# Performance work log

Measured on AMD Instinct MI355X. Metric: run time of the kernel, lower is better.

Reference implementation:

```python
import jax, jax.numpy as jnp
import numpy as np

D_MODEL = 1024
NUM_HEADS = 16
HEAD_DIM = D_MODEL // NUM_HEADS


def setup_inputs() -> dict:
    key = jax.random.key(0)
    ks = jax.random.split(key, 12)
    B, Lq, Lkv = 4, 1024, 2048
    s = 1.0 / np.sqrt(D_MODEL)
    inp = {
        "decoder_hidden": jax.random.normal(ks[0], (B, Lq, D_MODEL), jnp.float32),
        "encoder_hidden": jax.random.normal(ks[1], (B, Lkv, D_MODEL), jnp.float32),
        "encoder_mask": jnp.ones((B, 1, 1, Lkv), jnp.int32),
        "Wq": jax.random.normal(ks[2], (D_MODEL, D_MODEL), jnp.float32) * s,
        "bq": jnp.zeros((D_MODEL,), jnp.float32),
        "Wk": jax.random.normal(ks[3], (D_MODEL, D_MODEL), jnp.float32) * s,
        "bk": jnp.zeros((D_MODEL,), jnp.float32),
        "Wv": jax.random.normal(ks[4], (D_MODEL, D_MODEL), jnp.float32) * s,
        "bv": jnp.zeros((D_MODEL,), jnp.float32),
        "Wo": jax.random.normal(ks[5], (D_MODEL, D_MODEL), jnp.float32) * s,
        "bo": jnp.zeros((D_MODEL,), jnp.float32),
    }
    return inp


def _split_heads(x):
    # [B, L, D] -> [B, H, L, Dh]
    B, L, _ = x.shape
    return x.reshape(B, L, NUM_HEADS, HEAD_DIM).transpose(0, 2, 1, 3)


def reference(decoder_hidden, encoder_hidden, encoder_mask,
              Wq, bq, Wk, bk, Wv, bv, Wo, bo):
    B, Lq, _ = decoder_hidden.shape
    q = _split_heads(decoder_hidden @ Wq.T + bq)   # [B,H,Lq,Dh]
    k = _split_heads(encoder_hidden @ Wk.T + bk)   # [B,H,Lkv,Dh]
    v = _split_heads(encoder_hidden @ Wv.T + bv)   # [B,H,Lkv,Dh]
    scale = 1.0 / np.sqrt(HEAD_DIM).astype(np.float32)
    scores = jnp.einsum('bhqd,bhkd->bhqk', q, k) * scale  # [B,H,Lq,Lkv]
    scores = jnp.where(encoder_mask == 0, jnp.float32(-jnp.inf), scores)
    attn = jax.nn.softmax(scores, axis=-1)  # dropout is identity in eval mode
    out = jnp.einsum('bhqk,bhkd->bhqd', attn, v)  # [B,H,Lq,Dh]
    out = out.transpose(0, 2, 1, 3).reshape(B, Lq, D_MODEL)
    return out @ Wo.T + bo
```

## Files before the change

### kernel.cpp

```cpp
#include <hip/hip_runtime.h>
#include <hip/hip_bf16.h>
#include <stdint.h>
#include <math.h>

#define B_   4
#define H_   16
#define LQ_  1024
#define LKV_ 2048
#define DM_  1024
#define DH_  64

typedef __attribute__((ext_vector_type(8))) __bf16 bf16x8;
typedef __attribute__((ext_vector_type(4))) float  f32x4;
typedef __attribute__((ext_vector_type(16))) float f32x16;
typedef __attribute__((ext_vector_type(8))) short  short8;
typedef __attribute__((ext_vector_type(2))) unsigned uint2v;

__device__ __forceinline__ void gload_lds16(const void* g, void* l) {
  __builtin_amdgcn_global_load_lds(
      (const __attribute__((address_space(1))) void*)g,
      (__attribute__((address_space(3))) void*)l, 16, 0, 0);
}

__device__ __forceinline__ void drain_vmem() {
  asm volatile("s_waitcnt vmcnt(0)" ::: "memory");
  __builtin_amdgcn_sched_barrier(0);
}

#if __has_builtin(__builtin_amdgcn_exp2f)
__device__ __forceinline__ float EXP2(float x) { return __builtin_amdgcn_exp2f(x); }
#else
__device__ __forceinline__ float EXP2(float x) {
  float r; asm("v_exp_f32 %0, %1" : "=v"(r) : "v"(x)); return r;
}
#endif

#if __has_builtin(__builtin_amdgcn_permlane32_swap)
__device__ __forceinline__ void xswap(unsigned& a, unsigned& b) {
  uint2v r = __builtin_amdgcn_permlane32_swap(a, b, false, false);
  a = r[0]; b = r[1];
}
#else
__device__ __forceinline__ void xswap(unsigned& a, unsigned& b) {
  unsigned xa = (unsigned)__shfl_xor((int)a, 32);
  unsigned xb = (unsigned)__shfl_xor((int)b, 32);
  bool hi = (threadIdx.x & 32) != 0;
  unsigned na = hi ? xb : a;
  unsigned nb = hi ? b : xa;
  a = na; b = nb;
}
#endif

__device__ __forceinline__ unsigned pack2(float a, float b) {
  unsigned lo = (unsigned)__bfloat16_as_ushort(__float2bfloat16(a));
  unsigned hi = (unsigned)__bfloat16_as_ushort(__float2bfloat16(b));
  return lo | (hi << 16);
}

struct CastArgs {
  const float* src[6];
  __hip_bfloat16* dst[6];
  int n[6];
  const int* msk;
  __hip_bfloat16* mdst;
  int mn;
};

__global__ void cast_multi(CastArgs a) {
  int seg = blockIdx.y;
  int i = (blockIdx.x * blockDim.x + threadIdx.x) * 8;
  if (seg == 6) {
    if (i >= a.mn) return;
    const int* s = a.msk + i;
    union { short8 v; __hip_bfloat16 h[8]; } u;
#pragma unroll
    for (int j = 0; j < 8; ++j) u.h[j] = __float2bfloat16(s[j] ? 1.0f : 0.0f);
    *(short8*)(a.mdst + i) = u.v;
    return;
  }
  int n = a.n[seg];
  if (i >= n) return;
  const float* s = a.src[seg] + i;
  float4 x = *(const float4*)s;
  float4 y = *(const float4*)(s + 4);
  union { short8 v; __hip_bfloat16 h[8]; } u;
  u.h[0] = __float2bfloat16(x.x); u.h[1] = __float2bfloat16(x.y);
  u.h[2] = __float2bfloat16(x.z); u.h[3] = __float2bfloat16(x.w);
  u.h[4] = __float2bfloat16(y.x); u.h[5] = __float2bfloat16(y.y);
  u.h[6] = __float2bfloat16(y.z); u.h[7] = __float2bfloat16(y.w);
  *(short8*)(a.dst[seg] + i) = u.v;
}

template<int MODE>
__global__ __launch_bounds__(256, 3)
void gemm_bt(const __hip_bfloat16* __restrict__ A,
             const __hip_bfloat16* __restrict__ Bt,
             const float* __restrict__ bias,
             void* __restrict__ Cout, int M, int N, int K) {
  __shared__ __hip_bfloat16 lA[2][128 * 64];
  __shared__ __hip_bfloat16 lB[2][64 * 64];
  const int tid = threadIdx.x;
  const int lane = tid & 63, wv = tid >> 6;
  const int l16 = lane & 15, lg = lane >> 4;
  const int wm = wv >> 1, wn = wv & 1;
  const int xcd = blockIdx.x & 7, idx = blockIdx.x >> 3;
  const int tileM = (xcd * 4 + (idx >> 4)) * 128, tileN = (idx & 15) * 64;
  const int KB = K * 2;

  f32x4 acc[4][2] = {};
  const int o0 = wv * 1024 + lane * 16;

  auto GSTAGE = [&](int bi, int kt) {
#pragma unroll
    for (int j = 0; j < 4; ++j) {
      int o = o0 + j * 4096;
      int row = o >> 7, col = (o & 127) ^ ((row & 7) << 4);
      gload_lds16((const char*)A + (size_t)(tileM + row) * KB + kt * 2 + col,
                  (char*)lA[bi] + wv * 1024 + j * 4096);
    }
#pragma unroll
    for (int j = 0; j < 2; ++j) {
      int o = o0 + j * 4096;
      int row = o >> 7, col = (o & 127) ^ ((row & 7) << 4);
      gload_lds16((const char*)Bt + (size_t)(tileN + row) * KB + kt * 2 + col,
                  (char*)lB[bi] + wv * 1024 + j * 4096);
    }
  };

  GSTAGE(0, 0);
  drain_vmem();
  __syncthreads();
  int buf = 0;
  const int NT = K / 64;
  for (int t = 0; t < NT; ++t) {
    if (t + 1 < NT) GSTAGE(buf ^ 1, (t + 1) * 64);
    bf16x8 af[4][2], bfr[2][2];
#pragma unroll
    for (int mt = 0; mt < 4; ++mt) {
      const int row = wm * 64 + mt * 16 + l16;
      const int sw = (row & 7) << 4;
#pragma unroll
      for (int kk = 0; kk < 2; ++kk)
        af[mt][kk] = *(const bf16x8*)((const char*)lA[buf] + row * 128 + ((kk * 64 + lg * 16) ^ sw));
    }
#pragma unroll
    for (int nt = 0; nt < 2; ++nt) {
      const int row = wn * 32 + nt * 16 + l16;
      const int sw = (row & 7) << 4;
#pragma unroll
      for (int kk = 0; kk < 2; ++kk)
        bfr[nt][kk] = *(const bf16x8*)((const char*)lB[buf] + row * 128 + ((kk * 64 + lg * 16) ^ sw));
    }
#pragma unroll
    for (int kk = 0; kk < 2; ++kk)
#pragma unroll
      for (int mt = 0; mt < 4; ++mt)
#pragma unroll
        for (int nt = 0; nt < 2; ++nt)
          acc[mt][nt] = __builtin_amdgcn_mfma_f32_16x16x32_bf16(af[mt][kk], bfr[nt][kk], acc[mt][nt], 0, 0, 0);
    drain_vmem();
    __syncthreads();
    buf ^= 1;
  }

#pragma unroll
  for (int mt = 0; mt < 4; ++mt) {
#pragma unroll
    for (int nt = 0; nt < 2; ++nt) {
      int col = tileN + wn * 32 + nt * 16 + l16;
      float bcol = bias[col];
      int row0 = tileM + wm * 64 + mt * 16 + lg * 4;
      f32x4 a = acc[mt][nt];
#pragma unroll
      for (int r = 0; r < 4; ++r) {
        int row = row0 + r;
        float v = a[r] + bcol;
        if (MODE == 0) {
          ((__hip_bfloat16*)Cout)[(size_t)row * N + col] = __float2bfloat16(v);
        } else {
          ((float*)Cout)[(size_t)row * N + col] = v;
        }
      }
    }
  }
}

__global__ __launch_bounds__(256, 3)
void gemm_qkv(const __hip_bfloat16* __restrict__ decB,
              const __hip_bfloat16* __restrict__ WqB,
              const float* __restrict__ bq,
              const __hip_bfloat16* __restrict__ encB,
              const __hip_bfloat16* __restrict__ WkvB,
              const float* __restrict__ bk,
              const float* __restrict__ bv,
              __hip_bfloat16* __restrict__ Qout,
              __hip_bfloat16* __restrict__ Kout,
              __hip_bfloat16* __restrict__ Vtout,
              const int* __restrict__ vmask) {
  const int K = 1024;
  __shared__ __hip_bfloat16 ls[24576];
  __hip_bfloat16* lAp = ls;
  __hip_bfloat16* lBp = ls + 12288;
  const int tid = threadIdx.x;
  const int lane = tid & 63, wv = tid >> 6;
  const int l16 = lane & 15, lg = lane >> 4;
  const int wm = wv >> 1, wn = wv & 1;

  const int xcd = blockIdx.x & 7;
  const int idx = blockIdx.x >> 3;
  const bool isQ = idx < 32;
  int tileM, tileN;
  const __hip_bfloat16 *A, *Bt;
  if (isQ) {
    int qt = xcd * 32 + idx;
    tileM = (qt >> 3) * 128; tileN = (qt & 7) * 128;
    A = decB; Bt = WqB;
  } else {
    int kvt = xcd * 128 + (idx - 32);
    tileM = (kvt >> 4) * 128; tileN = (kvt & 15) * 128;
    A = encB; Bt = WkvB;
  }
  const int KB = K * 2;

  f32x4 acc[4][4] = {};
  const int o0 = tid * 16;

  auto GSTAGE = [&](int bi, int kt) {
#pragma unroll
    for (int j = 0; j < 2; ++j) {
      int o = o0 + j * 4096;
      int row = o >> 6, col = (o & 63) ^ ((row & 3) << 4);
      gload_lds16((const char*)A + (size_t)(tileM + row) * KB + kt * 2 + col,
                  (char*)(lAp + bi * 4096) + (tid & 192) * 16 + j * 4096);
    }
#pragma unroll
    for (int j = 0; j < 2; ++j) {
      int o = o0 + j * 4096;
      int row = o >> 6, col = (o & 63) ^ ((row & 3) << 4);
      gload_lds16((const char*)Bt + (size_t)(tileN + row) * KB + kt * 2 + col,
                  (char*)(lBp + bi * 4096) + (tid & 192) * 16 + j * 4096);
    }
  };

  GSTAGE(0, 0);
  GSTAGE(1, 32);
  const int NT = K / 32;
  for (int t = 0; t < NT; ++t) {
    if (t < NT - 1) {
      asm volatile("s_waitcnt vmcnt(4)" ::: "memory");
    } else {
      asm volatile("s_waitcnt vmcnt(0)" ::: "memory");
    }
    __builtin_amdgcn_sched_barrier(0);
    __syncthreads();
    if (t + 2 < NT) GSTAGE((t + 2) % 3, (t + 2) * 32);

    const int buf = t % 3;
    bf16x8 af[4], bfr[4];
#pragma unroll
    for (int mt = 0; mt < 4; ++mt) {
      const int row = wm * 64 + mt * 16 + l16;
      af[mt] = *(const bf16x8*)((const char*)(lAp + buf * 4096) + row * 64 + ((lg * 16) ^ ((row & 3) << 4)));
    }
#pragma unroll
    for (int nt = 0; nt < 4; ++nt) {
      const int row = wn * 64 + nt * 16 + l16;
      bfr[nt] = *(const bf16x8*)((const char*)(lBp + buf * 4096) + row * 64 + ((lg * 16) ^ ((row & 3) << 4)));
    }
#pragma unroll
    for (int mt = 0; mt < 4; ++mt)
#pragma unroll
      for (int nt = 0; nt < 4; ++nt)
        acc[mt][nt] = __builtin_amdgcn_mfma_f32_16x16x32_bf16(af[mt], bfr[nt], acc[mt][nt], 0, 0, 0);
  }

  if (!isQ && tileN >= 1024) {
    const int b0 = tileM >> 11;
    const int kvb = tileM & 2047;
    const int cvbase = tileN - 1024;
    __syncthreads();
#pragma unroll
    for (int mt = 0; mt < 4; ++mt) {
      int kvr0 = wm * 64 + mt * 16 + lg * 4;
#pragma unroll
      for (int nt = 0; nt < 4; ++nt) {
        int cvr = wn * 64 + nt * 16 + l16;
        float bc = bv[cvbase + cvr];
        f32x4 a = acc[mt][nt];
        union { unsigned u2[2]; __hip_bfloat16 h[4]; } pkv;
#pragma unroll
        for (int r = 0; r < 4; ++r) {
          float v = a[r] + bc;
          if (!vmask[b0 * 2048 + kvb + kvr0 + r]) v = 0.0f;
          pkv.h[r] = __float2bfloat16(v);
        }
        *(uint2v*)(ls + cvr * 132 + kvr0) = *(uint2v*)pkv.u2;
      }
    }
    __syncthreads();
#pragma unroll
    for (int p = 0; p < 32; ++p) {
      int row = wv + p * 4;
      unsigned d = *(const unsigned*)((const char*)ls + row * 264 + lane * 4);
      *(unsigned*)((char*)Vtout + (((size_t)(b0 * 1024 + cvbase + row)) * 2048 + kvb + lane * 2) * 2) = d;
    }
  } else {
#pragma unroll
    for (int mt = 0; mt < 4; ++mt) {
#pragma unroll
      for (int nt = 0; nt < 4; ++nt) {
        int col = tileN + wn * 64 + nt * 16 + l16;
        int row0 = tileM + wm * 64 + mt * 16 + lg * 4;
        f32x4 a = acc[mt][nt];
        if (isQ) {
          float bc = bq[col];
#pragma unroll
          for (int r = 0; r < 4; ++r) {
            int row = row0 + r;
            Qout[(size_t)row * 1024 + col] = __float2bfloat16(a[r] + bc);
          }
        } else {
          float bc = bk[col];
#pragma unroll
          for (int r = 0; r < 4; ++r) {
            int row = row0 + r;
            Kout[(size_t)row * 1024 + col] = __float2bfloat16(a[r] + bc);
          }
        }
      }
    }
  }
}

__global__ __launch_bounds__(256, 2)
void attn_fwd(const __hip_bfloat16* __restrict__ Qg,
              const __hip_bfloat16* __restrict__ Kg,
              const __hip_bfloat16* __restrict__ Vt,
              const __hip_bfloat16* __restrict__ mkb,
              __hip_bfloat16* __restrict__ AO) {
  __shared__ __hip_bfloat16 lK[2][128 * 64];
  __shared__ __hip_bfloat16 lV[2][2][64 * 64];
  const int tid = threadIdx.x, lane = tid & 63, wv = tid >> 6;
  const int l32 = lane & 31, h = lane >> 5;

  const int blk = blockIdx.x;
  const int c8 = blk & 7, j = blk >> 3;
  const int g8 = c8 * 8 + (j & 7);
  const int qi = j >> 3;
  const int hd = g8 & 15, b = g8 >> 4;
  const int qb = qi * 128;
  const int q0 = qb + wv * 32;

  const char* qbase = (const char*)Qg +
      ((size_t)(b * LQ_ + q0 + l32) * DM_ + hd * DH_ + h * 8) * 2;
  bf16x8 qf[4];
#pragma unroll
  for (int dk = 0; dk < 4; ++dk) qf[dk] = *(const bf16x8*)(qbase + dk * 32);

  f32x16 o_[2] = {};
  f32x16 l_acc = {};
  float m2 = -1e30f;
  const float S2 = 0.18033688f;
  const __hip_bfloat16* mrow = mkb + b * LKV_;
  const char* Kbase = (const char*)Kg + ((size_t)(b * LKV_) * DM_ + hd * DH_) * 2;
  const char* Vbase = (const char*)Vt + ((size_t)((b * H_ + hd) * DH_)) * LKV_ * 2;

  const int ofs = wv * 1024 + lane * 16;

  auto STAGE = [&](int bi, int kv0) {
#pragma unroll
    for (int r = 0; r < 4; ++r) {
      int o = ofs + r * 4096;
      int row = o >> 7, col = (o & 127) ^ ((row & 7) << 4);
      gload_lds16(Kbase + (size_t)(kv0 + row) * 2048 + col,
                  (char*)lK[bi] + wv * 1024 + r * 4096);
    }
#pragma unroll
    for (int s = 0; s < 2; ++s)
#pragma unroll
      for (int r = 0; r < 2; ++r) {
        int o = ofs + r * 4096;
        int row = o >> 7, col = (o & 127) ^ ((row & 7) << 4);
        gload_lds16(Vbase + (size_t)row * 4096 + (kv0 + s * 64) * 2 + col,
                    (char*)lV[bi][s] + wv * 1024 + r * 4096);
      }
  };

  STAGE(0, 0);
  drain_vmem();
  __syncthreads();
  int buf = 0;

  for (int it = 0; it < LKV_ / 128; ++it) {
    const int kv0 = it * 128;
    if (it + 1 < LKV_ / 128) STAGE(buf ^ 1, kv0 + 128);

    f32x16 z[4];
#pragma unroll
    for (int t = 0; t < 4; ++t) {
      z[t] = {};
      const int row = t * 32 + l32;
      const int sw = (row & 7) << 4;
      const char* kp = (const char*)lK[buf] + row * 128;
      __builtin_amdgcn_s_setprio(1);
#pragma unroll
      for (int dk = 0; dk < 4; ++dk) {
        bf16x8 kf = *(const bf16x8*)(kp + ((dk * 32 + h * 16) ^ sw));
        z[t] = __builtin_amdgcn_mfma_f32_32x32x16_bf16(kf, qf[dk], z[t], 0, 0, 0);
      }
      __builtin_amdgcn_s_setprio(0);
    }

    f32x16 zm;
#pragma unroll
    for (int g = 0; g < 16; ++g)
      zm[g] = fmaxf(fmaxf(z[0][g], z[1][g]), fmaxf(z[2][g], z[3][g]));
    float m0 = fmaxf(fmaxf(zm[0], zm[1]), fmaxf(zm[2], zm[3]));
    float m1 = fmaxf(fmaxf(zm[4], zm[5]), fmaxf(zm[6], zm[7]));
    float m4 = fmaxf(fmaxf(zm[8], zm[9]), fmaxf(zm[10], zm[11]));
    float m5 = fmaxf(fmaxf(zm[12], zm[13]), fmaxf(zm[14], zm[15]));
    float mx = fmaxf(fmaxf(m0, m1), fmaxf(m4, m5));
    mx = fmaxf(mx, __shfl_xor(mx, 32));
    float mx2 = mx * S2;

    if (!__all(mx2 - m2 <= 11.5416f)) {
      float mn = fmaxf(m2, mx2);
      float alpha = EXP2(m2 - mn);
      m2 = mn;
#pragma unroll
      for (int g = 0; g < 16; ++g) {
        float a2 = __shfl(alpha, (g & 3) + 8 * (g >> 2) + 4 * h);
        o_[0][g] *= a2;
        o_[1][g] *= a2;
        l_acc[g] *= a2;
      }
    }

    const float negm2 = -m2;
    unsigned pk[4][4][2];
#pragma unroll
    for (int t = 0; t < 4; ++t)
#pragma unroll
      for (int s = 0; s < 4; ++s) {
        float p0 = EXP2(fmaf(z[t][s * 4 + 0], S2, negm2));
        float p1 = EXP2(fmaf(z[t][s * 4 + 1], S2, negm2));
        float p2 = EXP2(fmaf(z[t][s * 4 + 2], S2, negm2));
        float p3 = EXP2(fmaf(z[t][s * 4 + 3], S2, negm2));
        pk[t][s][0] = pack2(p0, p1);
        pk[t][s][1] = pack2(p2, p3);
      }

#pragma unroll
    for (int c = 0; c < 8; ++c) {
      const int t = c >> 1, cc = c & 1;
      const int s = c >> 2, cl = c & 3;
      unsigned w0 = pk[t][2 * cc + 0][0], w1 = pk[t][2 * cc + 0][1];
      unsigned w2 = pk[t][2 * cc + 1][0], w3 = pk[t][2 * cc + 1][1];
      xswap(w0, w2);
      xswap(w1, w3);
      union { unsigned w[4]; bf16x8 v; } au;
      au.w[0] = w0; au.w[1] = w1; au.w[2] = w2; au.w[3] = w3;
      bf16x8 mb8 = *(const bf16x8*)(mrow + kv0 + c * 16 + h * 8);
      __builtin_amdgcn_s_setprio(1);
#pragma unroll
      for (int dt = 0; dt < 2; ++dt) {
        const int row = dt * 32 + l32;
        const int sw = (row & 7) << 4;
        bf16x8 vf = *(const bf16x8*)((const char*)lV[buf][s] + row * 128 + ((cl * 32 + h * 16) ^ sw));
        o_[dt] = __builtin_amdgcn_mfma_f32_32x32x16_bf16(au.v, vf, o_[dt], 0, 0, 0);
      }
      l_acc = __builtin_amdgcn_mfma_f32_32x32x16_bf16(au.v, mb8, l_acc, 0, 0, 0);
      __builtin_amdgcn_s_setprio(0);
    }
    drain_vmem();
    __syncthreads();
    buf ^= 1;
  }

#pragma unroll
  for (int dt = 0; dt < 2; ++dt)
#pragma unroll
    for (int g = 0; g < 16; ++g) {
      int q = (g & 3) + 8 * (g >> 2) + 4 * h;
      AO[(size_t)(b * LQ_ + qb + wv * 32 + q) * DM_ + hd * DH_ + dt * 32 + l32] =
          __float2bfloat16(o_[dt][g] / l_acc[g]);
    }
}

extern "C" void kernel_launch(void* const* d_in, const int* in_sizes, int n_in,
                              void* d_out, int out_size, void* d_ws, size_t ws_size,
                              hipStream_t stream) {
  const float* dec = (const float*)d_in[0];
  const float* enc = (const float*)d_in[1];
  const int*   msk = (const int*)d_in[2];
  const float* Wq = (const float*)d_in[3];
  const float* bq = (const float*)d_in[4];
  const float* Wk = (const float*)d_in[5];
  const float* bk = (const float*)d_in[6];
  const float* Wv = (const float*)d_in[7];
  const float* bv = (const float*)d_in[8];
  const float* Wo = (const float*)d_in[9];
  const float* bo = (const float*)d_in[10];

  char* ws = (char*)d_ws;
  __hip_bfloat16* decB = (__hip_bfloat16*)(ws);
  __hip_bfloat16* encB = (__hip_bfloat16*)(ws + 8388608);
  __hip_bfloat16* WqB  = (__hip_bfloat16*)(ws + 25165824);
  __hip_bfloat16* WkvB = (__hip_bfloat16*)(ws + 27262976);
  __hip_bfloat16* WoB  = (__hip_bfloat16*)(ws + 31457280);
  __hip_bfloat16* Qb   = (__hip_bfloat16*)(ws + 33554432);
  __hip_bfloat16* Kb   = (__hip_bfloat16*)(ws + 41943040);
  __hip_bfloat16* Vtb  = (__hip_bfloat16*)(ws + 58720256);
  __hip_bfloat16* AO   = (__hip_bfloat16*)(ws + 75497472);
  __hip_bfloat16* mk2  = (__hip_bfloat16*)(ws + 83886080);

  CastArgs ca;
  ca.src[0] = dec; ca.dst[0] = decB;             ca.n[0] = 4096 * 1024;
  ca.src[1] = enc; ca.dst[1] = encB;             ca.n[1] = 8192 * 1024;
  ca.src[2] = Wq;  ca.dst[2] = WqB;              ca.n[2] = 1024 * 1024;
  ca.src[3] = Wk;  ca.dst[3] = WkvB;             ca.n[3] = 1024 * 1024;
  ca.src[4] = Wv;  ca.dst[4] = WkvB + 1048576;   ca.n[4] = 1024 * 1024;
  ca.src[5] = Wo;  ca.dst[5] = WoB;              ca.n[5] = 1024 * 1024;
  ca.msk = msk; ca.mdst = mk2; ca.mn = B_ * LKV_;
  cast_multi<<<dim3(4096, 7), dim3(256), 0, stream>>>(ca);

  gemm_qkv<<<dim3(1280), dim3(256), 0, stream>>>(decB, WqB, bq, encB, WkvB, bk, bv,
                                                 Qb, Kb, Vtb, msk);

  attn_fwd<<<dim3(512), dim3(256), 0, stream>>>(Qb, Kb, Vtb, mk2, AO);

  gemm_bt<2><<<dim3(512), dim3(256), 0, stream>>>(AO, WoB, bo, d_out, 4096, 1024, 1024);
}
```

Baseline: 154.0 us.

## Split attention over KV halves with a separate merge kernel

```diff
diff --git a/kernel.cpp b/kernel.cpp
--- a/kernel.cpp
+++ b/kernel.cpp
@@ -332,24 +332,29 @@
   }
 }
 
-__global__ __launch_bounds__(256, 2)
-void attn_fwd(const __hip_bfloat16* __restrict__ Qg,
-              const __hip_bfloat16* __restrict__ Kg,
-              const __hip_bfloat16* __restrict__ Vt,
-              const __hip_bfloat16* __restrict__ mkb,
-              __hip_bfloat16* __restrict__ AO) {
-  __shared__ __hip_bfloat16 lK[2][128 * 64];
-  __shared__ __hip_bfloat16 lV[2][2][64 * 64];
+__global__ __launch_bounds__(256, 4)
+void attn_part(const __hip_bfloat16* __restrict__ Qg,
+               const __hip_bfloat16* __restrict__ Kg,
+               const __hip_bfloat16* __restrict__ Vt,
+               const __hip_bfloat16* __restrict__ mkb,
+               float* __restrict__ Opart,
+               float* __restrict__ Mpart,
+               float* __restrict__ Lpart) {
+  __shared__ __hip_bfloat16 lK[2][64 * 64];
+  __shared__ __hip_bfloat16 lV[2][64 * 64];
   const int tid = threadIdx.x, lane = tid & 63, wv = tid >> 6;
   const int l32 = lane & 31, h = lane >> 5;
 
   const int blk = blockIdx.x;
   const int c8 = blk & 7, j = blk >> 3;
   const int g8 = c8 * 8 + (j & 7);
-  const int qi = j >> 3;
+  const int rest = j >> 3;
+  const int qi = rest >> 1, kvh = rest & 1;
   const int hd = g8 & 15, b = g8 >> 4;
   const int qb = qi * 128;
   const int q0 = qb + wv * 32;
+  const int kvbase = kvh * 1024;
+  const int p = g8 * 16 + rest;
 
   const char* qbase = (const char*)Qg +
       ((size_t)(b * LQ_ + q0 + l32) * DM_ + hd * DH_ + h * 8) * 2;
@@ -366,38 +371,29 @@
   const char* Vbase = (const char*)Vt + ((size_t)((b * H_ + hd) * DH_)) * LKV_ * 2;
 
   const int ofs = wv * 1024 + lane * 16;
+  const int r0 = ofs >> 7, c0s = (ofs & 127) ^ ((r0 & 7) << 4);
+  const int ofs1 = ofs + 4096;
+  const int r1 = ofs1 >> 7, c1s = (ofs1 & 127) ^ ((r1 & 7) << 4);
 
   auto STAGE = [&](int bi, int kv0) {
-#pragma unroll
-    for (int r = 0; r < 4; ++r) {
-      int o = ofs + r * 4096;
-      int row = o >> 7, col = (o & 127) ^ ((row & 7) << 4);
-      gload_lds16(Kbase + (size_t)(kv0 + row) * 2048 + col,
-                  (char*)lK[bi] + wv * 1024 + r * 4096);
-    }
-#pragma unroll
-    for (int s = 0; s < 2; ++s)
-#pragma unroll
-      for (int r = 0; r < 2; ++r) {
-        int o = ofs + r * 4096;
-        int row = o >> 7, col = (o & 127) ^ ((row & 7) << 4);
-        gload_lds16(Vbase + (size_t)row * 4096 + (kv0 + s * 64) * 2 + col,
-                    (char*)lV[bi][s] + wv * 1024 + r * 4096);
-      }
+    gload_lds16(Kbase + (size_t)(kv0 + r0) * 2048 + c0s, (char*)lK[bi] + wv * 1024);
+    gload_lds16(Kbase + (size_t)(kv0 + r1) * 2048 + c1s, (char*)lK[bi] + 4096 + wv * 1024);
+    gload_lds16(Vbase + (size_t)r0 * 4096 + kv0 * 2 + c0s, (char*)lV[bi] + wv * 1024);
+    gload_lds16(Vbase + (size_t)r1 * 4096 + kv0 * 2 + c1s, (char*)lV[bi] + 4096 + wv * 1024);
   };
 
-  STAGE(0, 0);
+  STAGE(0, kvbase);
   drain_vmem();
   __syncthreads();
   int buf = 0;
 
-  for (int it = 0; it < LKV_ / 128; ++it) {
-    const int kv0 = it * 128;
-    if (it + 1 < LKV_ / 128) STAGE(buf ^ 1, kv0 + 128);
-
-    f32x16 z[4];
-#pragma unroll
-    for (int t = 0; t < 4; ++t) {
+  for (int it = 0; it < 16; ++it) {
+    const int kv0 = kvbase + it * 64;
+    if (it + 1 < 16) STAGE(buf ^ 1, kv0 + 64);
+
+    f32x16 z[2];
+#pragma unroll
+    for (int t = 0; t < 2; ++t) {
       z[t] = {};
       const int row = t * 32 + l32;
       const int sw = (row & 7) << 4;
@@ -413,8 +409,7 @@
 
     f32x16 zm;
 #pragma unroll
-    for (int g = 0; g < 16; ++g)
-      zm[g] = fmaxf(fmaxf(z[0][g], z[1][g]), fmaxf(z[2][g], z[3][g]));
+    for (int g = 0; g < 16; ++g) zm[g] = fmaxf(z[0][g], z[1][g]);
     float m0 = fmaxf(fmaxf(zm[0], zm[1]), fmaxf(zm[2], zm[3]));
     float m1 = fmaxf(fmaxf(zm[4], zm[5]), fmaxf(zm[6], zm[7]));
     float m4 = fmaxf(fmaxf(zm[8], zm[9]), fmaxf(zm[10], zm[11]));
@@ -437,9 +432,9 @@
     }
 
     const float negm2 = -m2;
-    unsigned pk[4][4][2];
-#pragma unroll
-    for (int t = 0; t < 4; ++t)
+    unsigned pk[2][4][2];
+#pragma unroll
+    for (int t = 0; t < 2; ++t)
 #pragma unroll
       for (int s = 0; s < 4; ++s) {
         float p0 = EXP2(fmaf(z[t][s * 4 + 0], S2, negm2));
@@ -451,9 +446,8 @@
       }
 
 #pragma unroll
-    for (int c = 0; c < 8; ++c) {
+    for (int c = 0; c < 4; ++c) {
       const int t = c >> 1, cc = c & 1;
-      const int s = c >> 2, cl = c & 3;
       unsigned w0 = pk[t][2 * cc + 0][0], w1 = pk[t][2 * cc + 0][1];
       unsigned w2 = pk[t][2 * cc + 1][0], w3 = pk[t][2 * cc + 1][1];
       xswap(w0, w2);
@@ -466,7 +460,7 @@
       for (int dt = 0; dt < 2; ++dt) {
         const int row = dt * 32 + l32;
         const int sw = (row & 7) << 4;
-        bf16x8 vf = *(const bf16x8*)((const char*)lV[buf][s] + row * 128 + ((cl * 32 + h * 16) ^ sw));
+        bf16x8 vf = *(const bf16x8*)((const char*)lV[buf] + row * 128 + ((c * 32 + h * 16) ^ sw));
         o_[dt] = __builtin_amdgcn_mfma_f32_32x32x16_bf16(au.v, vf, o_[dt], 0, 0, 0);
       }
       l_acc = __builtin_amdgcn_mfma_f32_32x32x16_bf16(au.v, mb8, l_acc, 0, 0, 0);
@@ -477,14 +471,61 @@
     buf ^= 1;
   }
 
+  float* Op = Opart + (size_t)p * 8192;
 #pragma unroll
   for (int dt = 0; dt < 2; ++dt)
 #pragma unroll
     for (int g = 0; g < 16; ++g) {
       int q = (g & 3) + 8 * (g >> 2) + 4 * h;
-      AO[(size_t)(b * LQ_ + qb + wv * 32 + q) * DM_ + hd * DH_ + dt * 32 + l32] =
-          __float2bfloat16(o_[dt][g] / l_acc[g]);
-    }
+      Op[(wv * 32 + q) * 64 + dt * 32 + l32] = o_[dt][g];
+    }
+  Mpart[p * 128 + wv * 32 + l32] = m2;
+#pragma unroll
+  for (int g = 0; g < 16; ++g) {
+    int q = (g & 3) + 8 * (g >> 2) + 4 * h;
+    Lpart[p * 128 + wv * 32 + q] = l_acc[g];
+  }
+}
+
+__global__ __launch_bounds__(256, 8)
+void attn_merge(const float* __restrict__ Opart,
+                const float* __restrict__ Mpart,
+                const float* __restrict__ Lpart,
+                __hip_bfloat16* __restrict__ AO) {
+  const int m = blockIdx.x;
+  const int g8 = m >> 3, qi = m & 7;
+  const int b = g8 >> 4, hd = g8 & 15;
+  const int p0 = m * 2, p1 = m * 2 + 1;
+  const int tid = threadIdx.x;
+  const int q = tid >> 1, d0 = (tid & 1) * 32;
+
+  float m0 = Mpart[p0 * 128 + q], m1 = Mpart[p1 * 128 + q];
+  float l0 = Lpart[p0 * 128 + q], l1 = Lpart[p1 * 128 + q];
+  float M = fmaxf(m0, m1);
+  float a0 = EXP2(m0 - M), a1 = EXP2(m1 - M);
+  float inv = 1.0f / (a0 * l0 + a1 * l1);
+  a0 *= inv; a1 *= inv;
+
+  const float* O0 = Opart + (size_t)p0 * 8192 + q * 64 + d0;
+  const float* O1 = Opart + (size_t)p1 * 8192 + q * 64 + d0;
+  __hip_bfloat16* dst = AO + (size_t)(b * LQ_ + qi * 128 + q) * DM_ + hd * DH_ + d0;
+#pragma unroll
+  for (int c = 0; c < 4; ++c) {
+    float4 x0 = *(const float4*)(O0 + c * 8);
+    float4 y0 = *(const float4*)(O0 + c * 8 + 4);
+    float4 x1 = *(const float4*)(O1 + c * 8);
+    float4 y1 = *(const float4*)(O1 + c * 8 + 4);
+    union { short8 v; __hip_bfloat16 h[8]; } u;
+    u.h[0] = __float2bfloat16(a0 * x0.x + a1 * x1.x);
+    u.h[1] = __float2bfloat16(a0 * x0.y + a1 * x1.y);
+    u.h[2] = __float2bfloat16(a0 * x0.z + a1 * x1.z);
+    u.h[3] = __float2bfloat16(a0 * x0.w + a1 * x1.w);
+    u.h[4] = __float2bfloat16(a0 * y0.x + a1 * y1.x);
+    u.h[5] = __float2bfloat16(a0 * y0.y + a1 * y1.y);
+    u.h[6] = __float2bfloat16(a0 * y0.z + a1 * y1.z);
+    u.h[7] = __float2bfloat16(a0 * y0.w + a1 * y1.w);
+    *(short8*)(dst + c * 8) = u.v;
+  }
 }
 
 extern "C" void kernel_launch(void* const* d_in, const int* in_sizes, int n_in,
@@ -507,12 +548,15 @@
   __hip_bfloat16* encB = (__hip_bfloat16*)(ws + 8388608);
   __hip_bfloat16* WqB  = (__hip_bfloat16*)(ws + 25165824);
   __hip_bfloat16* WkvB = (__hip_bfloat16*)(ws + 27262976);
-  __hip_bfloat16* WoB  = (__hip_bfloat16*)(ws + 31457280);
   __hip_bfloat16* Qb   = (__hip_bfloat16*)(ws + 33554432);
   __hip_bfloat16* Kb   = (__hip_bfloat16*)(ws + 41943040);
   __hip_bfloat16* Vtb  = (__hip_bfloat16*)(ws + 58720256);
   __hip_bfloat16* AO   = (__hip_bfloat16*)(ws + 75497472);
   __hip_bfloat16* mk2  = (__hip_bfloat16*)(ws + 83886080);
+  float* Mpart = (float*)(ws + 83902464);
+  float* Lpart = (float*)(ws + 84426752);
+  __hip_bfloat16* WoB  = (__hip_bfloat16*)(ws + 84951040);
+  float* Opart = (float*)(ws);
 
   CastArgs ca;
   ca.src[0] = dec; ca.dst[0] = decB;             ca.n[0] = 4096 * 1024;
@@ -527,7 +571,8 @@
   gemm_qkv<<<dim3(1280), dim3(256), 0, stream>>>(decB, WqB, bq, encB, WkvB, bk, bv,
                                                  Qb, Kb, Vtb, msk);
 
-  attn_fwd<<<dim3(512), dim3(256), 0, stream>>>(Qb, Kb, Vtb, mk2, AO);
+  attn_part<<<dim3(1024), dim3(256), 0, stream>>>(Qb, Kb, Vtb, mk2, Opart, Mpart, Lpart);
+  attn_merge<<<dim3(512), dim3(256), 0, stream>>>(Opart, Mpart, Lpart, AO);
 
   gemm_bt<2><<<dim3(512), dim3(256), 0, stream>>>(AO, WoB, bo, d_out, 4096, 1024, 1024);
 }
```

Measured after the change: 169.4 us. 10.0% more time.
